# Performance work log

Measured on AMD Instinct MI355X. Metric: run time of the kernel, lower is better.

## Reference

```python
import jax, jax.numpy as jnp
import numpy as np

D, H, L, DFF, V = 512, 8, 6, 2048, 32000
PAD = 0

def make_pe(max_len, d):
    pos = jnp.arange(max_len, dtype=jnp.float32)[:, None]
    div = jnp.exp(jnp.arange(0, d, 2, dtype=jnp.float32) * (-np.log(10000.0) / d))
    ang = pos * div  # [max_len, d/2]
    pe = jnp.zeros((max_len, d), jnp.float32)
    pe = pe.at[:, 0::2].set(jnp.sin(ang)).at[:, 1::2].set(jnp.cos(ang))
    return pe

def layernorm(x, g, b, eps=1e-5):
    m = x.mean(-1, keepdims=True)
    v = ((x - m) ** 2).mean(-1, keepdims=True)
    return (x - m) * jax.lax.rsqrt(v + eps) * g + b

def mha(q_in, k_in, v_in, W, Bv, mask):
    # W: [4, D, D] (q,k,v,out); Bv: [4, D]; mask broadcastable to [B,H,Tq,Tk] bool
    b, sq, d = q_in.shape
    hd = d // H
    def proj(x, w, bb):
        y = x @ w + bb
        return y.reshape(x.shape[0], x.shape[1], H, hd).transpose(0, 2, 1, 3)  # bhsd
    Q, K, Vh = proj(q_in, W[0], Bv[0]), proj(k_in, W[1], Bv[1]), proj(v_in, W[2], Bv[2])
    scores = jnp.einsum('bhqd,bhkd->bhqk', Q, K) / np.sqrt(hd).astype(np.float32)
    scores = jnp.where(mask, scores, jnp.float32(-1e9))
    attn = jax.nn.softmax(scores, axis=-1)
    ctx = jnp.einsum('bhqk,bhkd->bhqd', attn, Vh).transpose(0, 2, 1, 3).reshape(b, sq, d)
    return ctx @ W[3] + Bv[3]

def ffn(x, w1, b1, w2, b2):
    return jax.nn.relu(x @ w1 + b1) @ w2 + b2

def setup_inputs() -> dict:
    key = jax.random.key(0)
    ks = jax.random.split(key, 16)
    s = 0.02
    inp = {
        'src': jax.random.randint(ks[0], (8, 512), 0, V, dtype=jnp.int32),
        'tgt': jax.random.randint(ks[1], (8, 512), 0, V, dtype=jnp.int32),
        'src_emb': (jax.random.normal(ks[2], (V, D)) * s).at[PAD].set(0.0),
        'tgt_emb': (jax.random.normal(ks[3], (V, D)) * s).at[PAD].set(0.0),
        'enc_attn_w': jax.random.normal(ks[4], (L, 4, D, D)) * s,
        'enc_attn_b': jnp.zeros((L, 4, D)),
        'enc_ffn_w1': jax.random.normal(ks[5], (L, D, DFF)) * s,
        'enc_ffn_b1': jnp.zeros((L, DFF)),
        'enc_ffn_w2': jax.random.normal(ks[6], (L, DFF, D)) * s,
        'enc_ffn_b2': jnp.zeros((L, D)),
        'enc_ln_g': jnp.ones((L, 2, D)),
        'enc_ln_b': jnp.zeros((L, 2, D)),
        'dec_self_w': jax.random.normal(ks[7], (L, 4, D, D)) * s,
        'dec_self_b': jnp.zeros((L, 4, D)),
        'dec_cross_w': jax.random.normal(ks[8], (L, 4, D, D)) * s,
        'dec_cross_b': jnp.zeros((L, 4, D)),
        'dec_ffn_w1': jax.random.normal(ks[9], (L, D, DFF)) * s,
        'dec_ffn_b1': jnp.zeros((L, DFF)),
        'dec_ffn_w2': jax.random.normal(ks[10], (L, DFF, D)) * s,
        'dec_ffn_b2': jnp.zeros((L, D)),
        'dec_ln_g': jnp.ones((L, 3, D)),
        'dec_ln_b': jnp.zeros((L, 3, D)),
        'out_w': jax.random.normal(ks[11], (D, V)) * s,
        'out_b': jnp.zeros((V,)),
    }
    return inp

def reference(src, tgt, src_emb, tgt_emb, enc_attn_w, enc_attn_b, enc_ffn_w1, enc_ffn_b1,
              enc_ffn_w2, enc_ffn_b2, enc_ln_g, enc_ln_b, dec_self_w, dec_self_b,
              dec_cross_w, dec_cross_b, dec_ffn_w1, dec_ffn_b1, dec_ffn_w2, dec_ffn_b2,
              dec_ln_g, dec_ln_b, out_w, out_b):
    B_, S = src.shape
    T = tgt.shape[1]
    pe = make_pe(max(S, T), D)
    scale = jnp.float32(np.sqrt(D))

    src_pad = (src != PAD)[:, None, None, :]                    # [B,1,1,S]
    causal = jnp.tril(jnp.ones((T, T), bool))                   # [T,T]
    tgt_mask = (tgt != PAD)[:, None, None, :] & causal[None, None]  # [B,1,T,T]

    # encoder (dropout = identity at inference)
    x = src_emb[src] * scale + pe[None, :S]
    for i in range(L):
        a = mha(x, x, x, enc_attn_w[i], enc_attn_b[i], src_pad)
        x = layernorm(x + a, enc_ln_g[i, 0], enc_ln_b[i, 0])
        f = ffn(x, enc_ffn_w1[i], enc_ffn_b1[i], enc_ffn_w2[i], enc_ffn_b2[i])
        x = layernorm(x + f, enc_ln_g[i, 1], enc_ln_b[i, 1])
    memory = x

    # decoder
    y = tgt_emb[tgt] * scale + pe[None, :T]
    for i in range(L):
        a = mha(y, y, y, dec_self_w[i], dec_self_b[i], tgt_mask)
        y = layernorm(y + a, dec_ln_g[i, 0], dec_ln_b[i, 0])
        c = mha(y, memory, memory, dec_cross_w[i], dec_cross_b[i], src_pad)
        y = layernorm(y + c, dec_ln_g[i, 1], dec_ln_b[i, 1])
        f = ffn(y, dec_ffn_w1[i], dec_ffn_b1[i], dec_ffn_w2[i], dec_ffn_b2[i])
        y = layernorm(y + f, dec_ln_g[i, 2], dec_ln_b[i, 2])

    return y @ out_w + out_b  # [B, T, tgt_vocab]
```

## Files before the change

### kernel.cpp

```cpp
#include <hip/hip_runtime.h>
#include <hip/hip_bf16.h>


#define Dm 512
#define Hh 8
#define HD 64
#define Ll 6
#define DFFv 2048
#define Vv 32000
#define Bb 8
#define Ss 512
#define NTOK (Bb * Ss)
#define NROWC ((size_t)NTOK * Dm)

typedef __bf16 bf16x8 __attribute__((ext_vector_type(8)));
typedef __bf16 bf16x4 __attribute__((ext_vector_type(4)));
typedef float  f32x4  __attribute__((ext_vector_type(4)));

#define GLOAD16(gp, lp) __builtin_amdgcn_global_load_lds( \
    (const __attribute__((address_space(1))) unsigned int*)(const void*)(gp), \
    (__attribute__((address_space(3))) unsigned int*)(void*)(lp), 16, 0, 0)

__global__ void embed_pe_k(const int* __restrict__ tok, const float* __restrict__ emb,
                           float* __restrict__ out, __bf16* __restrict__ outb, int Slen)
{
    int row = blockIdx.x;
    int s = row % Slen;
    int t = tok[row];
    const float* e = emb + (size_t)t * Dm;
    float* o = out + (size_t)row * Dm;
    __bf16* ob = outb + (size_t)row * Dm;
    for (int dd = threadIdx.x; dd < Dm; dd += blockDim.x) {
        int j = dd >> 1;
        float div = expf((float)(2 * j) * (-9.210340371976184f / 512.0f));
        float ang = (float)s * div;
        float pe = (dd & 1) ? cosf(ang) : sinf(ang);
        float v = e[dd] * 22.627416997969522f + pe;
        o[dd] = v;
        ob[dd] = (__bf16)v;
    }
}

__global__ __launch_bounds__(256) void wtr_k(const float* __restrict__ W,
                                             __bf16* __restrict__ Wt, int K, int N)
{
    __shared__ float t[32][33];
    size_t msz = (size_t)K * N;
    const float* Wm = W + (size_t)blockIdx.z * msz;
    __bf16* Wtm = Wt + (size_t)blockIdx.z * msz;
    int n0 = blockIdx.x * 32, k0 = blockIdx.y * 32;
    int r = threadIdx.x >> 3, c4 = (threadIdx.x & 7) * 4;
    float4 v = *reinterpret_cast<const float4*>(&Wm[(size_t)(k0 + r) * N + n0 + c4]);
    t[r][c4] = v.x; t[r][c4 + 1] = v.y; t[r][c4 + 2] = v.z; t[r][c4 + 3] = v.w;
    __syncthreads();
    int n = threadIdx.x >> 3, kq = (threadIdx.x & 7) * 4;
    bf16x4 o;
    o[0] = (__bf16)t[kq + 0][n]; o[1] = (__bf16)t[kq + 1][n];
    o[2] = (__bf16)t[kq + 2][n]; o[3] = (__bf16)t[kq + 3][n];
    *reinterpret_cast<bf16x4*>(&Wtm[(size_t)(n0 + n) * K + k0 + kq]) = o;
}

template<int BM, int BN, int RELU, int MODE>
__global__ __launch_bounds__(256) void gemm_mfma_k(const __bf16* __restrict__ A,
                                                   const __bf16* __restrict__ Wt,
                                                   const float* __restrict__ bias,
                                                   void* __restrict__ Cout,
                                                   __bf16* __restrict__ out_k,
                                                   __bf16* __restrict__ out_vT,
                                                   int M, int N, int K)
{
    constexpr int NF_M = BM / 32;
    constexpr int NF_N = BN / 32;
    __shared__ __bf16 As[2][BM * 64];
    __shared__ __bf16 Bs[2][BN * 64];
    const int tid = threadIdx.x;
    const int wave = tid >> 6, lane = tid & 63;
    const int wr = wave >> 1, wc = wave & 1;
    const int row0 = blockIdx.y * BM, col0 = blockIdx.x * BN;

    f32x4 acc[NF_M][NF_N] = {};
    const int fr = lane & 15;
    const int kg = lane >> 4;

    auto stage = [&](int buf, int k0) {
        #pragma unroll
        for (int cc = 0; cc < BM / 32; ++cc) {
            int g = cc * 256 + tid;
            int r = g >> 3, gs = (g & 7) ^ (r & 7);
            GLOAD16(A + (size_t)(row0 + r) * K + k0 + gs * 8, &As[buf][g * 8]);
        }
        #pragma unroll
        for (int cc = 0; cc < BN / 32; ++cc) {
            int g = cc * 256 + tid;
            int r = g >> 3, gs = (g & 7) ^ (r & 7);
            int c = col0 + r;
            size_t wrow;
            if constexpr (MODE == 4)
                wrow = (size_t)(c >> 10) * 2048 + 512 + (c & 1023);
            else
                wrow = (size_t)c;
            GLOAD16(Wt + wrow * K + k0 + gs * 8, &Bs[buf][g * 8]);
        }
    };

    stage(0, 0);
    __syncthreads();

    const int nk = K >> 6;
    for (int kb = 0; kb < nk; ++kb) {
        int cur = kb & 1;
        if (kb + 1 < nk) stage(cur ^ 1, (kb + 1) * 64);

        const char* Ab  = (const char*)As[cur];
        const char* Bbp = (const char*)Bs[cur];
        #pragma unroll
        for (int ks = 0; ks < 2; ++ks) {
            bf16x8 af[NF_M], bq[NF_N];
            #pragma unroll
            for (int m = 0; m < NF_M; ++m) {
                int ar = wr * (BM / 2) + m * 16 + fr;
                af[m] = *reinterpret_cast<const bf16x8*>(
                    Ab + ar * 128 + (((ks * 4 + kg) ^ (ar & 7)) << 4));
            }
            #pragma unroll
            for (int n = 0; n < NF_N; ++n) {
                int br = wc * (BN / 2) + n * 16 + fr;
                bq[n] = *reinterpret_cast<const bf16x8*>(
                    Bbp + br * 128 + (((ks * 4 + kg) ^ (br & 7)) << 4));
            }
            #pragma unroll
            for (int m = 0; m < NF_M; ++m)
                #pragma unroll
                for (int n = 0; n < NF_N; ++n)
                    acc[m][n] = __builtin_amdgcn_mfma_f32_16x16x32_bf16(
                        af[m], bq[n], acc[m][n], 0, 0, 0);
        }
        __syncthreads();
    }

    #pragma unroll
    for (int m = 0; m < NF_M; ++m) {
        #pragma unroll
        for (int n = 0; n < NF_N; ++n) {
            int colg = col0 + wc * (BN / 2) + n * 16 + fr;
            float bv;
            if constexpr (MODE == 4)
                bv = bias[(colg >> 10) * 2048 + 512 + (colg & 1023)];
            else
                bv = bias[colg];
            #pragma unroll
            for (int j = 0; j < 4; ++j) {
                int row = row0 + wr * (BM / 2) + m * 16 + kg * 4 + j;
                float v = acc[m][n][j] + bv;
                if (RELU) v = fmaxf(v, 0.f);
                if constexpr (MODE == 0) {
                    ((float*)Cout)[(size_t)row * N + colg] = v;
                } else if constexpr (MODE == 1) {
                    ((__bf16*)Cout)[(size_t)row * N + colg] = (__bf16)v;
                } else if constexpr (MODE == 2) {
                    int seg = colg >> 9;
                    int c = colg & 511;
                    if (seg == 0) {
                        ((__bf16*)Cout)[(size_t)row * 512 + c] = (__bf16)v;
                    } else if (seg == 1) {
                        out_k[(size_t)row * 512 + c] = (__bf16)v;
                    } else {
                        int bi = row >> 9, sI = row & 511;
                        int hh = c >> 6, f = c & 63;
                        out_vT[(size_t)((bi * 8 + hh) * 64 + f) * 512 + sI] = (__bf16)v;
                    }
                } else {
                    int li = colg >> 10;
                    int cw = colg & 1023;
                    if (cw < 512) {
                        out_k[li * NROWC + (size_t)row * 512 + cw] = (__bf16)v;
                    } else {
                        int hh = (cw - 512) >> 6, f = (cw - 512) & 63;
                        int bi = row >> 9, sI = row & 511;
                        out_vT[li * NROWC +
                               (size_t)((bi * 8 + hh) * 64 + f) * 512 + sI] = (__bf16)v;
                    }
                }
            }
        }
    }
}

__global__ __launch_bounds__(512) void gemm256_k(const __bf16* __restrict__ A,
                                                 const __bf16* __restrict__ Wt,
                                                 const float* __restrict__ bias,
                                                 float* __restrict__ C,
                                                 int M, int N, int K)
{
    __shared__ __bf16 As[2][256 * 64];
    __shared__ __bf16 Bs[2][256 * 64];
    const int tid = threadIdx.x;
    const int wave = tid >> 6, lane = tid & 63;
    const int wr = wave >> 2, wc = wave & 3;
    const int row0 = blockIdx.x * 256, col0 = blockIdx.y * 256;

    f32x4 acc[8][4] = {};
    const int fr = lane & 15;
    const int kg = lane >> 4;

    auto stage = [&](int buf, int k0) {
        #pragma unroll
        for (int cc = 0; cc < 4; ++cc) {
            int g = cc * 512 + tid;
            int r = g >> 3, gs = (g & 7) ^ (r & 7);
            GLOAD16(A + (size_t)(row0 + r) * K + k0 + gs * 8, &As[buf][g * 8]);
        }
        #pragma unroll
        for (int cc = 0; cc < 4; ++cc) {
            int g = cc * 512 + tid;
            int r = g >> 3, gs = (g & 7) ^ (r & 7);
            GLOAD16(Wt + (size_t)(col0 + r) * K + k0 + gs * 8, &Bs[buf][g * 8]);
        }
    };

    stage(0, 0);
    __syncthreads();

    const int nk = K >> 6;
    for (int kb = 0; kb < nk; ++kb) {
        int cur = kb & 1;
        if (kb + 1 < nk) stage(cur ^ 1, (kb + 1) * 64);

        const char* Ab  = (const char*)As[cur];
        const char* Bbp = (const char*)Bs[cur];
        #pragma unroll
        for (int ks = 0; ks < 2; ++ks) {
            bf16x8 af[8], bq[4];
            #pragma unroll
            for (int m = 0; m < 8; ++m) {
                int ar = wr * 128 + m * 16 + fr;
                af[m] = *reinterpret_cast<const bf16x8*>(
                    Ab + ar * 128 + (((ks * 4 + kg) ^ (ar & 7)) << 4));
            }
            #pragma unroll
            for (int n = 0; n < 4; ++n) {
                int br = wc * 64 + n * 16 + fr;
                bq[n] = *reinterpret_cast<const bf16x8*>(
                    Bbp + br * 128 + (((ks * 4 + kg) ^ (br & 7)) << 4));
            }
            #pragma unroll
            for (int m = 0; m < 8; ++m)
                #pragma unroll
                for (int n = 0; n < 4; ++n)
                    acc[m][n] = __builtin_amdgcn_mfma_f32_16x16x32_bf16(
                        af[m], bq[n], acc[m][n], 0, 0, 0);
        }
        __syncthreads();
    }

    #pragma unroll
    for (int m = 0; m < 8; ++m) {
        #pragma unroll
        for (int n = 0; n < 4; ++n) {
            int colg = col0 + wc * 64 + n * 16 + fr;
            float bv = bias[colg];
            #pragma unroll
            for (int j = 0; j < 4; ++j) {
                int row = row0 + wr * 128 + m * 16 + kg * 4 + j;
                C[(size_t)row * N + colg] = acc[m][n][j] + bv;
            }
        }
    }
}

__global__ __launch_bounds__(256) void attn_mfma_k(const __bf16* __restrict__ Qb,
                                                   const __bf16* __restrict__ Kb,
                                                   const __bf16* __restrict__ VbT,
                                                   __bf16* __restrict__ Ob,
                                                   const int* __restrict__ key_tok,
                                                   int causal)
{
    __shared__ __bf16 Ks[2][128 * 64];
    __shared__ __bf16 Vs[2][64 * 128];
    __shared__ __bf16 Pl[4][16 * 128];

    const int tid = threadIdx.x;
    const int w = tid >> 6, lane = tid & 63;
    const int fr = lane & 15, kg = lane >> 4;
    const int q0 = blockIdx.x * 64;
    const int h = blockIdx.y, b = blockIdx.z;
    const int qrow = q0 + w * 16 + fr;
    const int swz = (fr & 7) << 4;

    bf16x8 qf[2];
    {
        const __bf16* qp = Qb + ((size_t)(b * 512 + qrow) * 512 + h * 64 + kg * 8);
        qf[0] = *reinterpret_cast<const bf16x8*>(qp);
        qf[1] = *reinterpret_cast<const bf16x8*>(qp + 32);
    }

    f32x4 po[4] = {};
    float m_run = -3.0e38f, l_run = 0.f;
    __bf16* pw = Pl[w];

    auto stage = [&](int buf, int kk0) {
        #pragma unroll
        for (int c = 0; c < 4; ++c) {
            int ch = c * 256 + tid;
            int r = ch >> 3, gsk = (ch & 7) ^ (r & 7);
            GLOAD16(Kb + ((size_t)(b * 512 + kk0 + r) * 512 + h * 64 + gsk * 8),
                    &Ks[buf][ch * 8]);
            int f = ch >> 4, gsv = (ch & 15) ^ (f & 7);
            GLOAD16(VbT + ((size_t)((b * 8 + h) * 64 + f) * 512 + kk0 + gsv * 8),
                    &Vs[buf][ch * 8]);
        }
    };

    const int kkend = causal ? ((q0 + 64 + 127) & ~127) : 512;
    stage(0, 0);
    __syncthreads();

    for (int kk0 = 0; kk0 < kkend; kk0 += 128) {
        int cur = (kk0 >> 7) & 1;
        if (kk0 + 128 < kkend) stage(cur ^ 1, kk0 + 128);

        unsigned long long vm0 = __ballot(key_tok[b * 512 + kk0 + lane] != 0);
        unsigned long long vm1 = __ballot(key_tok[b * 512 + kk0 + 64 + lane] != 0);

        f32x4 st[8];
        #pragma unroll
        for (int kt = 0; kt < 8; ++kt) {
            f32x4 s = {};
            #pragma unroll
            for (int ks = 0; ks < 2; ++ks) {
                int byte = ((kt * 16 + fr) * 128 + ks * 64 + kg * 16) ^ swz;
                bf16x8 kf = *reinterpret_cast<const bf16x8*>((const char*)Ks[cur] + byte);
                s = __builtin_amdgcn_mfma_f32_16x16x32_bf16(kf, qf[ks], s, 0, 0, 0);
            }
            st[kt] = s;
        }

        float sv[8][4];
        float mloc = -3.0e38f;
        #pragma unroll
        for (int kt = 0; kt < 8; ++kt) {
            unsigned long long vm = (kt < 4) ? vm0 : vm1;
            #pragma unroll
            for (int j = 0; j < 4; ++j) {
                int kl = kt * 16 + kg * 4 + j;
                float s = st[kt][j] * 0.125f;
                bool ok = (vm >> (kl & 63)) & 1ull;
                if (causal && (kk0 + kl > qrow)) ok = false;
                s = ok ? s : -1e9f;
                sv[kt][j] = s;
                mloc = fmaxf(mloc, s);
            }
        }
        mloc = fmaxf(mloc, __shfl_xor(mloc, 16));
        mloc = fmaxf(mloc, __shfl_xor(mloc, 32));
        float m_new = fmaxf(m_run, mloc);
        float scale = __expf(m_run - m_new);
        float ls = 0.f;
        #pragma unroll
        for (int kt = 0; kt < 8; ++kt)
            #pragma unroll
            for (int j = 0; j < 4; ++j) {
                float p = __expf(sv[kt][j] - m_new);
                sv[kt][j] = p;
                ls += p;
            }
        ls += __shfl_xor(ls, 16);
        ls += __shfl_xor(ls, 32);
        l_run = l_run * scale + ls;
        m_run = m_new;

        #pragma unroll
        for (int kt = 0; kt < 8; ++kt)
            #pragma unroll
            for (int c = 0; c < 2; ++c) {
                union { __bf16 hh[2]; unsigned u; } pk;
                pk.hh[0] = (__bf16)sv[kt][2 * c];
                pk.hh[1] = (__bf16)sv[kt][2 * c + 1];
                int byte = (fr * 256 + kt * 32 + kg * 8 + c * 4) ^ swz;
                *reinterpret_cast<unsigned*>((char*)pw + byte) = pk.u;
            }

        {
            int qb4 = kg * 4;
            float s0 = __shfl(scale, qb4 + 0), s1 = __shfl(scale, qb4 + 1);
            float s2 = __shfl(scale, qb4 + 2), s3 = __shfl(scale, qb4 + 3);
            #pragma unroll
            for (int nf = 0; nf < 4; ++nf) {
                po[nf][0] *= s0; po[nf][1] *= s1;
                po[nf][2] *= s2; po[nf][3] *= s3;
            }
        }

        #pragma unroll
        for (int ks2 = 0; ks2 < 4; ++ks2) {
            int pbyte = (fr * 256 + ks2 * 64 + kg * 16) ^ swz;
            bf16x8 pa = *reinterpret_cast<const bf16x8*>((const char*)pw + pbyte);
            #pragma unroll
            for (int nf = 0; nf < 4; ++nf) {
                int vbyte = ((nf * 16 + fr) * 256 + ks2 * 64 + kg * 16) ^ swz;
                bf16x8 vf = *reinterpret_cast<const bf16x8*>((const char*)Vs[cur] + vbyte);
                po[nf] = __builtin_amdgcn_mfma_f32_16x16x32_bf16(pa, vf, po[nf], 0, 0, 0);
            }
        }
        __syncthreads();
    }

    {
        int qb4 = kg * 4;
        float r0 = 1.0f / __shfl(l_run, qb4 + 0);
        float r1 = 1.0f / __shfl(l_run, qb4 + 1);
        float r2 = 1.0f / __shfl(l_run, qb4 + 2);
        float r3 = 1.0f / __shfl(l_run, qb4 + 3);
        #pragma unroll
        for (int nf = 0; nf < 4; ++nf) {
            size_t base = (size_t)(b * 512 + q0 + w * 16 + qb4) * 512 + h * 64 + nf * 16 + fr;
            Ob[base]           = (__bf16)(po[nf][0] * r0);
            Ob[base + 512]     = (__bf16)(po[nf][1] * r1);
            Ob[base + 1024]    = (__bf16)(po[nf][2] * r2);
            Ob[base + 1536]    = (__bf16)(po[nf][3] * r3);
        }
    }
}

__global__ __launch_bounds__(256) void add_ln_k(float* __restrict__ x,
                                                const float* __restrict__ a,
                                                const float* __restrict__ g,
                                                const float* __restrict__ bb,
                                                __bf16* __restrict__ xb)
{
    int row = blockIdx.x;
    size_t base = (size_t)row * Dm;
    int tid = threadIdx.x;
    float v0 = x[base + tid]       + a[base + tid];
    float v1 = x[base + tid + 256] + a[base + tid + 256];
    float s  = v0 + v1;
    float s2 = v0 * v0 + v1 * v1;
    #pragma unroll
    for (int o = 1; o < 64; o <<= 1) {
        s  += __shfl_xor(s, o);
        s2 += __shfl_xor(s2, o);
    }
    __shared__ float red[8];
    int wid = tid >> 6, lane = tid & 63;
    if (lane == 0) { red[wid] = s; red[wid + 4] = s2; }
    __syncthreads();
    s  = red[0] + red[1] + red[2] + red[3];
    s2 = red[4] + red[5] + red[6] + red[7];
    float mean = s * (1.0f / 512.0f);
    float var  = s2 * (1.0f / 512.0f) - mean * mean;
    float rstd = rsqrtf(var + 1e-5f);
    float y0 = (v0 - mean) * rstd * g[tid]       + bb[tid];
    float y1 = (v1 - mean) * rstd * g[tid + 256] + bb[tid + 256];
    x[base + tid]        = y0;
    x[base + tid + 256]  = y1;
    xb[base + tid]       = (__bf16)y0;
    xb[base + tid + 256] = (__bf16)y1;
}

extern "C" void kernel_launch(void* const* d_in, const int* in_sizes, int n_in,
                              void* d_out, int out_size, void* d_ws, size_t ws_size,
                              hipStream_t stream)
{
    const int*   src        = (const int*)  d_in[0];
    const int*   tgt        = (const int*)  d_in[1];
    const float* src_emb    = (const float*)d_in[2];
    const float* tgt_emb    = (const float*)d_in[3];
    const float* enc_attn_w = (const float*)d_in[4];
    const float* enc_attn_b = (const float*)d_in[5];
    const float* enc_ffn_w1 = (const float*)d_in[6];
    const float* enc_ffn_b1 = (const float*)d_in[7];
    const float* enc_ffn_w2 = (const float*)d_in[8];
    const float* enc_ffn_b2 = (const float*)d_in[9];
    const float* enc_ln_g   = (const float*)d_in[10];
    const float* enc_ln_b   = (const float*)d_in[11];
    const float* dec_self_w = (const float*)d_in[12];
    const float* dec_self_b = (const float*)d_in[13];
    const float* dec_cross_w= (const float*)d_in[14];
    const float* dec_cross_b= (const float*)d_in[15];
    const float* dec_ffn_w1 = (const float*)d_in[16];
    const float* dec_ffn_b1 = (const float*)d_in[17];
    const float* dec_ffn_w2 = (const float*)d_in[18];
    const float* dec_ffn_b2 = (const float*)d_in[19];
    const float* dec_ln_g   = (const float*)d_in[20];
    const float* dec_ln_b   = (const float*)d_in[21];
    const float* out_w      = (const float*)d_in[22];
    const float* out_b      = (const float*)d_in[23];

    const size_t NROW = NROWC;
    const size_t NH1  = (size_t)NTOK * DFFv;

    float* ws  = (float*)d_ws;
    float* xe  = ws;
    float* xd  = xe + NROW;
    float* t0  = xd + NROW;

    __bf16* xeb  = (__bf16*)(t0 + NROW);
    __bf16* xdb  = xeb + NROW;
    __bf16* qbb  = xdb + NROW;
    __bf16* kbb  = qbb + NROW;
    __bf16* vbT  = kbb + NROW;
    __bf16* ctxb = vbT + NROW;
    __bf16* h1b  = ctxb + NROW;
    __bf16* kbb6 = h1b + NH1;
    __bf16* vbT6 = kbb6 + 6 * NROW;

    const size_t WSZ  = (size_t)Dm * Dm;
    const size_t FSZ  = (size_t)Dm * DFFv;
    __bf16* w_enc_attn = vbT6 + 6 * NROW;
    __bf16* w_enc_f1   = w_enc_attn + 24 * WSZ;
    __bf16* w_enc_f2   = w_enc_f1 + 6 * FSZ;
    __bf16* w_dec_self = w_enc_f2 + 6 * FSZ;
    __bf16* w_dec_cross= w_dec_self + 24 * WSZ;
    __bf16* w_dec_f1   = w_dec_cross + 24 * WSZ;
    __bf16* w_dec_f2   = w_dec_f1 + 6 * FSZ;
    __bf16* w_out      = w_dec_f2 + 6 * FSZ;

    wtr_k<<<dim3(Dm / 32, Dm / 32, 24), 256, 0, stream>>>(enc_attn_w, w_enc_attn, Dm, Dm);
    wtr_k<<<dim3(DFFv / 32, Dm / 32, 6), 256, 0, stream>>>(enc_ffn_w1, w_enc_f1, Dm, DFFv);
    wtr_k<<<dim3(Dm / 32, DFFv / 32, 6), 256, 0, stream>>>(enc_ffn_w2, w_enc_f2, DFFv, Dm);
    wtr_k<<<dim3(Dm / 32, Dm / 32, 24), 256, 0, stream>>>(dec_self_w, w_dec_self, Dm, Dm);
    wtr_k<<<dim3(Dm / 32, Dm / 32, 24), 256, 0, stream>>>(dec_cross_w, w_dec_cross, Dm, Dm);
    wtr_k<<<dim3(DFFv / 32, Dm / 32, 6), 256, 0, stream>>>(dec_ffn_w1, w_dec_f1, Dm, DFFv);
    wtr_k<<<dim3(Dm / 32, DFFv / 32, 6), 256, 0, stream>>>(dec_ffn_w2, w_dec_f2, DFFv, Dm);
    wtr_k<<<dim3(Vv / 32, Dm / 32, 1), 256, 0, stream>>>(out_w, w_out, Dm, Vv);

    auto gqkv = [&](const __bf16* A, const __bf16* Wt, const float* bias) {
        gemm_mfma_k<64, 128, 0, 2><<<dim3(1536 / 128, NTOK / 64), 256, 0, stream>>>(
            A, Wt, bias, qbb, kbb, vbT, NTOK, 1536, Dm);
    };
    auto g64f = [&](const __bf16* A, const __bf16* Wt, const float* bias, float* C, int K) {
        gemm_mfma_k<64, 64, 0, 0><<<dim3(Dm / 64, NTOK / 64), 256, 0, stream>>>(
            A, Wt, bias, C, nullptr, nullptr, NTOK, Dm, K);
    };
    auto g64b = [&](const __bf16* A, const __bf16* Wt, const float* bias, __bf16* C, int K) {
        gemm_mfma_k<64, 64, 0, 1><<<dim3(Dm / 64, NTOK / 64), 256, 0, stream>>>(
            A, Wt, bias, C, nullptr, nullptr, NTOK, Dm, K);
    };
    auto attn = [&](const __bf16* Q, const __bf16* K, const __bf16* Vt, __bf16* O,
                    const int* kt, int causal) {
        attn_mfma_k<<<dim3(Ss / 64, Hh, Bb), 256, 0, stream>>>(Q, K, Vt, O, kt, causal);
    };
    auto lnorm = [&](float* x, const float* a, const float* g, const float* b, __bf16* xb) {
        add_ln_k<<<NTOK, 256, 0, stream>>>(x, a, g, b, xb);
    };

    embed_pe_k<<<NTOK, 256, 0, stream>>>(src, src_emb, xe, xeb, Ss);
    embed_pe_k<<<NTOK, 256, 0, stream>>>(tgt, tgt_emb, xd, xdb, Ss);

    for (int i = 0; i < Ll; ++i) {
        const __bf16* W = w_enc_attn + (size_t)i * 4 * WSZ;
        const float* Bv = enc_attn_b + (size_t)i * 4 * Dm;
        gqkv(xeb, W, Bv);
        attn(qbb, kbb, vbT, ctxb, src, 0);
        g64f(ctxb, W + 3 * WSZ, Bv + 3 * Dm, t0, Dm);
        lnorm(xe, t0, enc_ln_g + i * 2 * Dm, enc_ln_b + i * 2 * Dm, xeb);
        gemm_mfma_k<128, 128, 1, 1><<<dim3(DFFv / 128, NTOK / 128), 256, 0, stream>>>(
            xeb, w_enc_f1 + (size_t)i * FSZ, enc_ffn_b1 + i * DFFv, h1b, nullptr, nullptr,
            NTOK, DFFv, Dm);
        g64f(h1b, w_enc_f2 + (size_t)i * FSZ, enc_ffn_b2 + i * Dm, t0, DFFv);
        lnorm(xe, t0, enc_ln_g + i * 2 * Dm + Dm, enc_ln_b + i * 2 * Dm + Dm, xeb);
    }

    gemm_mfma_k<64, 128, 0, 4><<<dim3(6144 / 128, NTOK / 64), 256, 0, stream>>>(
        xeb, w_dec_cross, dec_cross_b, nullptr, kbb6, vbT6, NTOK, 6144, Dm);

    for (int i = 0; i < Ll; ++i) {
        const __bf16* Wsf = w_dec_self + (size_t)i * 4 * WSZ;
        const float* Bsf = dec_self_b + (size_t)i * 4 * Dm;
        gqkv(xdb, Wsf, Bsf);
        attn(qbb, kbb, vbT, ctxb, tgt, 1);
        g64f(ctxb, Wsf + 3 * WSZ, Bsf + 3 * Dm, t0, Dm);
        lnorm(xd, t0, dec_ln_g + i * 3 * Dm, dec_ln_b + i * 3 * Dm, xdb);

        const __bf16* Wc = w_dec_cross + (size_t)i * 4 * WSZ;
        const float* Bc = dec_cross_b + (size_t)i * 4 * Dm;
        g64b(xdb, Wc + 0 * WSZ, Bc + 0 * Dm, qbb, Dm);
        attn(qbb, kbb6 + (size_t)i * NROW, vbT6 + (size_t)i * NROW, ctxb, src, 0);
        g64f(ctxb, Wc + 3 * WSZ, Bc + 3 * Dm, t0, Dm);
        lnorm(xd, t0, dec_ln_g + i * 3 * Dm + Dm, dec_ln_b + i * 3 * Dm + Dm, xdb);

        gemm_mfma_k<128, 128, 1, 1><<<dim3(DFFv / 128, NTOK / 128), 256, 0, stream>>>(
            xdb, w_dec_f1 + (size_t)i * FSZ, dec_ffn_b1 + i * DFFv, h1b, nullptr, nullptr,
            NTOK, DFFv, Dm);
        g64f(h1b, w_dec_f2 + (size_t)i * FSZ, dec_ffn_b2 + i * Dm, t0, DFFv);
        lnorm(xd, t0, dec_ln_g + i * 3 * Dm + 2 * Dm, dec_ln_b + i * 3 * Dm + 2 * Dm, xdb);
    }

    gemm256_k<<<dim3(NTOK / 256, Vv / 256), 512, 0, stream>>>(
        xdb, w_out, out_b, (float*)d_out, NTOK, Vv, Dm);
}
```

Measured before the change: 2.121 ms.

## Keep residual stream in bf16 and vectorize add+layernorm per wavefront

The fp32 residual copies (xe, xd, t0) are removed, so the residual stream and the GEMM outputs that feed layernorm are now stored only as bf16. Add+LayerNorm is rewritten to give each row to one wavefront with 8-wide bf16 vector loads, and the shared-memory reduction and block barrier are dropped. Embedding for source and target is merged into one launch. This cuts memory traffic in the memory-bound elementwise kernels and the GEMM epilogues, but rounding the residual to bf16 at every layer can lower accuracy across the 12 layers.

```diff
diff --git a/kernel.cpp b/kernel.cpp
--- a/kernel.cpp
+++ b/kernel.cpp
@@ -21,23 +21,23 @@
     (const __attribute__((address_space(1))) unsigned int*)(const void*)(gp), \
     (__attribute__((address_space(3))) unsigned int*)(void*)(lp), 16, 0, 0)
 
-__global__ void embed_pe_k(const int* __restrict__ tok, const float* __restrict__ emb,
-                           float* __restrict__ out, __bf16* __restrict__ outb, int Slen)
+__global__ void embed_pe_k(const int* __restrict__ tok_s, const int* __restrict__ tok_t,
+                           const float* __restrict__ emb_s, const float* __restrict__ emb_t,
+                           __bf16* __restrict__ out_s, __bf16* __restrict__ out_t)
 {
     int row = blockIdx.x;
-    int s = row % Slen;
+    int s = row & 511;
+    const int* tok = blockIdx.y ? tok_t : tok_s;
+    const float* emb = blockIdx.y ? emb_t : emb_s;
+    __bf16* ob = (blockIdx.y ? out_t : out_s) + (size_t)row * Dm;
     int t = tok[row];
     const float* e = emb + (size_t)t * Dm;
-    float* o = out + (size_t)row * Dm;
-    __bf16* ob = outb + (size_t)row * Dm;
     for (int dd = threadIdx.x; dd < Dm; dd += blockDim.x) {
         int j = dd >> 1;
         float div = expf((float)(2 * j) * (-9.210340371976184f / 512.0f));
         float ang = (float)s * div;
         float pe = (dd & 1) ? cosf(ang) : sinf(ang);
-        float v = e[dd] * 22.627416997969522f + pe;
-        o[dd] = v;
-        ob[dd] = (__bf16)v;
+        ob[dd] = (__bf16)(e[dd] * 22.627416997969522f + pe);
     }
 }
 
@@ -153,9 +153,7 @@
                 int row = row0 + wr * (BM / 2) + m * 16 + kg * 4 + j;
                 float v = acc[m][n][j] + bv;
                 if (RELU) v = fmaxf(v, 0.f);
-                if constexpr (MODE == 0) {
-                    ((float*)Cout)[(size_t)row * N + colg] = v;
-                } else if constexpr (MODE == 1) {
+                if constexpr (MODE == 1) {
                     ((__bf16*)Cout)[(size_t)row * N + colg] = (__bf16)v;
                 } else if constexpr (MODE == 2) {
                     int seg = colg >> 9;
@@ -422,39 +420,43 @@
     }
 }
 
-__global__ __launch_bounds__(256) void add_ln_k(float* __restrict__ x,
-                                                const float* __restrict__ a,
-                                                const float* __restrict__ g,
-                                                const float* __restrict__ bb,
-                                                __bf16* __restrict__ xb)
-{
-    int row = blockIdx.x;
-    size_t base = (size_t)row * Dm;
-    int tid = threadIdx.x;
-    float v0 = x[base + tid]       + a[base + tid];
-    float v1 = x[base + tid + 256] + a[base + tid + 256];
-    float s  = v0 + v1;
-    float s2 = v0 * v0 + v1 * v1;
+__global__ __launch_bounds__(256) void add_ln_b_k(__bf16* __restrict__ xb,
+                                                  const __bf16* __restrict__ ab,
+                                                  const float* __restrict__ g,
+                                                  const float* __restrict__ bb)
+{
+    const int w = threadIdx.x >> 6, lane = threadIdx.x & 63;
+    const int row = blockIdx.x * 4 + w;
+    const size_t base = (size_t)row * Dm + lane * 8;
+    bf16x8 xv = *reinterpret_cast<const bf16x8*>(&xb[base]);
+    bf16x8 av = *reinterpret_cast<const bf16x8*>(&ab[base]);
+    float v[8];
+    float s = 0.f, s2 = 0.f;
+    #pragma unroll
+    for (int j = 0; j < 8; ++j) {
+        v[j] = (float)xv[j] + (float)av[j];
+        s += v[j];
+        s2 += v[j] * v[j];
+    }
     #pragma unroll
     for (int o = 1; o < 64; o <<= 1) {
         s  += __shfl_xor(s, o);
         s2 += __shfl_xor(s2, o);
     }
-    __shared__ float red[8];
-    int wid = tid >> 6, lane = tid & 63;
-    if (lane == 0) { red[wid] = s; red[wid + 4] = s2; }
-    __syncthreads();
-    s  = red[0] + red[1] + red[2] + red[3];
-    s2 = red[4] + red[5] + red[6] + red[7];
     float mean = s * (1.0f / 512.0f);
     float var  = s2 * (1.0f / 512.0f) - mean * mean;
     float rstd = rsqrtf(var + 1e-5f);
-    float y0 = (v0 - mean) * rstd * g[tid]       + bb[tid];
-    float y1 = (v1 - mean) * rstd * g[tid + 256] + bb[tid + 256];
-    x[base + tid]        = y0;
-    x[base + tid + 256]  = y1;
-    xb[base + tid]       = (__bf16)y0;
-    xb[base + tid + 256] = (__bf16)y1;
+    float4 g0 = *reinterpret_cast<const float4*>(&g[lane * 8]);
+    float4 g1 = *reinterpret_cast<const float4*>(&g[lane * 8 + 4]);
+    float4 b0 = *reinterpret_cast<const float4*>(&bb[lane * 8]);
+    float4 b1 = *reinterpret_cast<const float4*>(&bb[lane * 8 + 4]);
+    float gv[8] = {g0.x, g0.y, g0.z, g0.w, g1.x, g1.y, g1.z, g1.w};
+    float bv[8] = {b0.x, b0.y, b0.z, b0.w, b1.x, b1.y, b1.z, b1.w};
+    bf16x8 yv;
+    #pragma unroll
+    for (int j = 0; j < 8; ++j)
+        yv[j] = (__bf16)((v[j] - mean) * rstd * gv[j] + bv[j]);
+    *reinterpret_cast<bf16x8*>(&xb[base]) = yv;
 }
 
 extern "C" void kernel_launch(void* const* d_in, const int* in_sizes, int n_in,
@@ -489,14 +491,10 @@
     const size_t NROW = NROWC;
     const size_t NH1  = (size_t)NTOK * DFFv;
 
-    float* ws  = (float*)d_ws;
-    float* xe  = ws;
-    float* xd  = xe + NROW;
-    float* t0  = xd + NROW;
-
-    __bf16* xeb  = (__bf16*)(t0 + NROW);
+    __bf16* xeb  = (__bf16*)d_ws;
     __bf16* xdb  = xeb + NROW;
-    __bf16* qbb  = xdb + NROW;
+    __bf16* t0b  = xdb + NROW;
+    __bf16* qbb  = t0b + NROW;
     __bf16* kbb  = qbb + NROW;
     __bf16* vbT  = kbb + NROW;
     __bf16* ctxb = vbT + NROW;
@@ -528,10 +526,6 @@
         gemm_mfma_k<64, 128, 0, 2><<<dim3(1536 / 128, NTOK / 64), 256, 0, stream>>>(
             A, Wt, bias, qbb, kbb, vbT, NTOK, 1536, Dm);
     };
-    auto g64f = [&](const __bf16* A, const __bf16* Wt, const float* bias, float* C, int K) {
-        gemm_mfma_k<64, 64, 0, 0><<<dim3(Dm / 64, NTOK / 64), 256, 0, stream>>>(
-            A, Wt, bias, C, nullptr, nullptr, NTOK, Dm, K);
-    };
     auto g64b = [&](const __bf16* A, const __bf16* Wt, const float* bias, __bf16* C, int K) {
         gemm_mfma_k<64, 64, 0, 1><<<dim3(Dm / 64, NTOK / 64), 256, 0, stream>>>(
             A, Wt, bias, C, nullptr, nullptr, NTOK, Dm, K);
@@ -540,25 +534,24 @@
                     const int* kt, int causal) {
         attn_mfma_k<<<dim3(Ss / 64, Hh, Bb), 256, 0, stream>>>(Q, K, Vt, O, kt, causal);
     };
-    auto lnorm = [&](float* x, const float* a, const float* g, const float* b, __bf16* xb) {
-        add_ln_k<<<NTOK, 256, 0, stream>>>(x, a, g, b, xb);
-    };
-
-    embed_pe_k<<<NTOK, 256, 0, stream>>>(src, src_emb, xe, xeb, Ss);
-    embed_pe_k<<<NTOK, 256, 0, stream>>>(tgt, tgt_emb, xd, xdb, Ss);
+    auto lnorm = [&](__bf16* xb, const __bf16* ab, const float* g, const float* b) {
+        add_ln_b_k<<<NTOK / 4, 256, 0, stream>>>(xb, ab, g, b);
+    };
+
+    embed_pe_k<<<dim3(NTOK, 2), 256, 0, stream>>>(src, tgt, src_emb, tgt_emb, xeb, xdb);
 
     for (int i = 0; i < Ll; ++i) {
         const __bf16* W = w_enc_attn + (size_t)i * 4 * WSZ;
         const float* Bv = enc_attn_b + (size_t)i * 4 * Dm;
         gqkv(xeb, W, Bv);
         attn(qbb, kbb, vbT, ctxb, src, 0);
-        g64f(ctxb, W + 3 * WSZ, Bv + 3 * Dm, t0, Dm);
-        lnorm(xe, t0, enc_ln_g + i * 2 * Dm, enc_ln_b + i * 2 * Dm, xeb);
+        g64b(ctxb, W + 3 * WSZ, Bv + 3 * Dm, t0b, Dm);
+        lnorm(xeb, t0b, enc_ln_g + i * 2 * Dm, enc_ln_b + i * 2 * Dm);
         gemm_mfma_k<128, 128, 1, 1><<<dim3(DFFv / 128, NTOK / 128), 256, 0, stream>>>(
             xeb, w_enc_f1 + (size_t)i * FSZ, enc_ffn_b1 + i * DFFv, h1b, nullptr, nullptr,
             NTOK, DFFv, Dm);
-        g64f(h1b, w_enc_f2 + (size_t)i * FSZ, enc_ffn_b2 + i * Dm, t0, DFFv);
-        lnorm(xe, t0, enc_ln_g + i * 2 * Dm + Dm, enc_ln_b + i * 2 * Dm + Dm, xeb);
+        g64b(h1b, w_enc_f2 + (size_t)i * FSZ, enc_ffn_b2 + i * Dm, t0b, DFFv);
+        lnorm(xeb, t0b, enc_ln_g + i * 2 * Dm + Dm, enc_ln_b + i * 2 * Dm + Dm);
     }
 
     gemm_mfma_k<64, 128, 0, 4><<<dim3(6144 / 128, NTOK / 64), 256, 0, stream>>>(
@@ -569,21 +562,21 @@
         const float* Bsf = dec_self_b + (size_t)i * 4 * Dm;
         gqkv(xdb, Wsf, Bsf);
         attn(qbb, kbb, vbT, ctxb, tgt, 1);
-        g64f(ctxb, Wsf + 3 * WSZ, Bsf + 3 * Dm, t0, Dm);
-        lnorm(xd, t0, dec_ln_g + i * 3 * Dm, dec_ln_b + i * 3 * Dm, xdb);
+        g64b(ctxb, Wsf + 3 * WSZ, Bsf + 3 * Dm, t0b, Dm);
+        lnorm(xdb, t0b, dec_ln_g + i * 3 * Dm, dec_ln_b + i * 3 * Dm);
 
         const __bf16* Wc = w_dec_cross + (size_t)i * 4 * WSZ;
         const float* Bc = dec_cross_b + (size_t)i * 4 * Dm;
         g64b(xdb, Wc + 0 * WSZ, Bc + 0 * Dm, qbb, Dm);
         attn(qbb, kbb6 + (size_t)i * NROW, vbT6 + (size_t)i * NROW, ctxb, src, 0);
-        g64f(ctxb, Wc + 3 * WSZ, Bc + 3 * Dm, t0, Dm);
-        lnorm(xd, t0, dec_ln_g + i * 3 * Dm + Dm, dec_ln_b + i * 3 * Dm + Dm, xdb);
+        g64b(ctxb, Wc + 3 * WSZ, Bc + 3 * Dm, t0b, Dm);
+        lnorm(xdb, t0b, dec_ln_g + i * 3 * Dm + Dm, dec_ln_b + i * 3 * Dm + Dm);
 
         gemm_mfma_k<128, 128, 1, 1><<<dim3(DFFv / 128, NTOK / 128), 256, 0, stream>>>(
             xdb, w_dec_f1 + (size_t)i * FSZ, dec_ffn_b1 + i * DFFv, h1b, nullptr, nullptr,
             NTOK, DFFv, Dm);
-        g64f(h1b, w_dec_f2 + (size_t)i * FSZ, dec_ffn_b2 + i * Dm, t0, DFFv);
-        lnorm(xd, t0, dec_ln_g + i * 3 * Dm + 2 * Dm, dec_ln_b + i * 3 * Dm + 2 * Dm, xdb);
+        g64b(h1b, w_dec_f2 + (size_t)i * FSZ, dec_ffn_b2 + i * Dm, t0b, DFFv);
+        lnorm(xdb, t0b, dec_ln_g + i * 3 * Dm + 2 * Dm, dec_ln_b + i * 3 * Dm + 2 * Dm);
     }
 
     gemm256_k<<<dim3(NTOK / 256, Vv / 256), 512, 0, stream>>>(
```

Result: faster. 1.983 ms (-6.5%).
